# Kernel optimization log

Measured on AMD Instinct MI355X. Metric: run time of the kernel, lower is better.

## Reference

```python
import jax, jax.numpy as jnp
import numpy as np

N, IN_F, H, D = 3072, 512, 8, 64


def setup_inputs() -> dict:
    key = jax.random.key(0)
    k1, k2, k3, k4, k5 = jax.random.split(key, 5)
    x = jax.random.normal(k1, (N, IN_F), dtype=jnp.float32)
    adj = jax.random.randint(k2, (N, N), 0, 2, dtype=jnp.int32)
    # xavier-uniform-like scales
    s_W = (6.0 / (IN_F + H * D)) ** 0.5
    s_a = (6.0 / (H + D)) ** 0.5
    W = jax.random.uniform(k3, (H * D, IN_F), dtype=jnp.float32, minval=-s_W, maxval=s_W)
    a_src = jax.random.uniform(k4, (H, D), dtype=jnp.float32, minval=-s_a, maxval=s_a)
    a_dst = jax.random.uniform(k5, (H, D), dtype=jnp.float32, minval=-s_a, maxval=s_a)
    return {"x": x, "adj": adj, "W": W, "a_src": a_src, "a_dst": a_dst}


def reference(x, adj, W, a_src, a_dst):
    n = x.shape[0]
    Hh, d = a_src.shape
    h = (x @ W.T).reshape(n, Hh, d)                      # [n, H, d]
    e_src = jnp.einsum('nhd,hd->nh', h, a_src)           # [n, H]
    e_dst = jnp.einsum('nhd,hd->nh', h, a_dst)           # [n, H]
    e = e_src[:, None, :] + e_dst[None, :, :]            # [n, n, H], e[i,j]=src_i+dst_j
    e = jax.nn.leaky_relu(e, negative_slope=0.2)
    mask = (adj + jnp.eye(n, dtype=adj.dtype)) > 0       # [n, n]
    e = jnp.where(mask[:, :, None], e, -jnp.inf)
    alpha = jax.nn.softmax(e, axis=1)                    # softmax over j (neighbors)
    # out[i,h,d] = sum_j alpha[i,j,h] * h[j,h,d]  (dropout=0 / eval mode)
    out = jnp.einsum('ijh,jhd->ihd', alpha, h)
    return out.reshape(n, Hh * d)                        # concat=True
```

## Files before the change

kernel.cpp:

```cpp
#include <hip/hip_runtime.h>
#include <hip/hip_bf16.h>

typedef __bf16 bf16x8 __attribute__((ext_vector_type(8)));
typedef _Float16 half8 __attribute__((ext_vector_type(8)));
typedef _Float16 half2v __attribute__((ext_vector_type(2)));
typedef short s16x2 __attribute__((ext_vector_type(2)));
typedef float f32x4 __attribute__((ext_vector_type(4)));
typedef float f32x16 __attribute__((ext_vector_type(16)));

#define NROW 3072
#define NF 512
#define NH 8
#define ND 64
#define BP_BLOCKS 768
#define GEMM_BLOCKS 384

__device__ __forceinline__ unsigned gat_enc_key(float f) {
    unsigned u = __float_as_uint(f);
    return (f < 0.f) ? ~u : (u | 0x80000000u);
}
__device__ __forceinline__ float gat_dec_key(unsigned k) {
    unsigned u = (k & 0x80000000u) ? (k ^ 0x80000000u) : ~k;
    return __uint_as_float(u);
}

__device__ __forceinline__ bf16x8 gat_ld_cvt8(const float* p) {
    float4 f0 = *reinterpret_cast<const float4*>(p);
    float4 f1 = *reinterpret_cast<const float4*>(p + 4);
    bf16x8 o = { (__bf16)f0.x, (__bf16)f0.y, (__bf16)f0.z, (__bf16)f0.w,
                 (__bf16)f1.x, (__bf16)f1.y, (__bf16)f1.z, (__bf16)f1.w };
    return o;
}

__global__ __launch_bounds__(256) void gat_gemm_bp(const float* __restrict__ x,
                                                   const float* __restrict__ W,
                                                   _Float16* __restrict__ hT,
                                                   const int* __restrict__ adj,
                                                   unsigned long long* __restrict__ bits64,
                                                   const float* __restrict__ a_src,
                                                   const float* __restrict__ a_dst,
                                                   float* __restrict__ e_srcT,
                                                   float* __restrict__ e_dstT,
                                                   unsigned* __restrict__ maxkey) {
    __shared__ __align__(16) _Float16 smem[10240];
    __shared__ float ered[2][2][2][32];

    int tid = threadIdx.x;
    int wave = tid >> 6;
    int lane = tid & 63;

    if (blockIdx.x < BP_BLOCKS) {
        int row = blockIdx.x * 4 + wave;
        const int* p = adj + (long)row * NROW + lane;
        int v[48];
#pragma unroll
        for (int s = 0; s < 48; ++s) v[s] = p[s * 64];
        unsigned long long diag = 1ull << (row & 63);
        int dseg = row >> 6;
#pragma unroll
        for (int s = 0; s < 48; ++s) {
            unsigned long long bal = __ballot(v[s] > 0);
            if (s == dseg) bal |= diag;
            if (lane == 0) bits64[(long)row * 48 + s] = bal;
        }
        return;
    }

    int b = blockIdx.x - BP_BLOCKS;
    int i0 = (b >> 3) * 64;
    int o0 = (b & 7) * 64;
    int head = b & 7;
    int half = lane >> 5;
    int l31 = lane & 31;
    int wr = wave >> 1;
    int wc = wave & 1;

    __bf16* sA = reinterpret_cast<__bf16*>(smem);
    __bf16* sB = reinterpret_cast<__bf16*>(smem) + 5120;

    int r = tid >> 2;
    int pp = tid & 3;
    const float* gA = x + (i0 + r) * NF + pp * 8;
    const float* gB = W + (o0 + r) * NF + pp * 8;
    int dslot = r * 40 + pp * 8;

    bf16x8 pA0, pB0, pA1, pB1;
    pA0 = gat_ld_cvt8(gA);
    pB0 = gat_ld_cvt8(gB);
    *reinterpret_cast<bf16x8*>(sA + dslot) = pA0;
    *reinterpret_cast<bf16x8*>(sB + dslot) = pB0;
    pA1 = gat_ld_cvt8(gA + 32);
    pB1 = gat_ld_cvt8(gB + 32);
    __syncthreads();

    f32x16 acc = {};
    int arow = (wr * 32 + l31) * 40;
    int brow = (wc * 32 + l31) * 40;

#pragma unroll
    for (int cc = 0; cc < 8; ++cc) {
        int c0 = cc * 2;
        if (c0 + 2 < 16) {
            pA0 = gat_ld_cvt8(gA + (c0 + 2) * 32);
            pB0 = gat_ld_cvt8(gB + (c0 + 2) * 32);
        }
        {
            const __bf16* pa = sA;
            const __bf16* pb = sB;
#pragma unroll
            for (int ks = 0; ks < 2; ++ks) {
                int q = (((ks << 1) | half)) << 3;
                bf16x8 a = *reinterpret_cast<const bf16x8*>(pa + arow + q);
                bf16x8 bb = *reinterpret_cast<const bf16x8*>(pb + brow + q);
                acc = __builtin_amdgcn_mfma_f32_32x32x16_bf16(a, bb, acc, 0, 0, 0);
            }
        }
        *reinterpret_cast<bf16x8*>(sA + 2560 + dslot) = pA1;
        *reinterpret_cast<bf16x8*>(sB + 2560 + dslot) = pB1;
        __syncthreads();

        int c1 = c0 + 1;
        if (c1 + 2 < 16) {
            pA1 = gat_ld_cvt8(gA + (c1 + 2) * 32);
            pB1 = gat_ld_cvt8(gB + (c1 + 2) * 32);
        }
        {
            const __bf16* pa = sA + 2560;
            const __bf16* pb = sB + 2560;
#pragma unroll
            for (int ks = 0; ks < 2; ++ks) {
                int q = (((ks << 1) | half)) << 3;
                bf16x8 a = *reinterpret_cast<const bf16x8*>(pa + arow + q);
                bf16x8 bb = *reinterpret_cast<const bf16x8*>(pb + brow + q);
                acc = __builtin_amdgcn_mfma_f32_32x32x16_bf16(a, bb, acc, 0, 0, 0);
            }
        }
        if (c1 + 1 < 16) {
            *reinterpret_cast<bf16x8*>(sA + dslot) = pA0;
            *reinterpret_cast<bf16x8*>(sB + dslot) = pB0;
        }
        __syncthreads();
    }

    _Float16* tt = smem + wave * 1280;
#pragma unroll
    for (int reg = 0; reg < 16; ++reg) {
        int rowl = (reg & 3) + 8 * (reg >> 2) + 4 * half;
        tt[rowl * 40 + l31] = (_Float16)acc[reg];
    }
    int orow = lane >> 1;
    int li = (lane & 1) * 16;
    half8 h0, h1;
#pragma unroll
    for (int t = 0; t < 8; ++t) h0[t] = tt[(li + t) * 40 + orow];
#pragma unroll
    for (int t = 0; t < 8; ++t) h1[t] = tt[(li + 8 + t) * 40 + orow];
    _Float16* op = hT + (long)(o0 + wc * 32 + orow) * NROW + i0 + wr * 32 + li;
    *reinterpret_cast<half8*>(op) = h0;
    *reinterpret_cast<half8*>(op + 8) = h1;

    half8 hv0 = *reinterpret_cast<const half8*>(tt + l31 * 40 + half * 16);
    half8 hv1 = *reinterpret_cast<const half8*>(tt + l31 * 40 + half * 16 + 8);
    const float* ap = a_src + head * ND + wc * 32 + half * 16;
    const float* dp = a_dst + head * ND + wc * 32 + half * 16;
    float4 as0 = *reinterpret_cast<const float4*>(ap);
    float4 as1 = *reinterpret_cast<const float4*>(ap + 4);
    float4 as2 = *reinterpret_cast<const float4*>(ap + 8);
    float4 as3 = *reinterpret_cast<const float4*>(ap + 12);
    float4 ad0 = *reinterpret_cast<const float4*>(dp);
    float4 ad1 = *reinterpret_cast<const float4*>(dp + 4);
    float4 ad2 = *reinterpret_cast<const float4*>(dp + 8);
    float4 ad3 = *reinterpret_cast<const float4*>(dp + 12);
    float ps = 0.f, pd = 0.f;
    ps += (float)hv0[0]*as0.x + (float)hv0[1]*as0.y + (float)hv0[2]*as0.z + (float)hv0[3]*as0.w;
    ps += (float)hv0[4]*as1.x + (float)hv0[5]*as1.y + (float)hv0[6]*as1.z + (float)hv0[7]*as1.w;
    ps += (float)hv1[0]*as2.x + (float)hv1[1]*as2.y + (float)hv1[2]*as2.z + (float)hv1[3]*as2.w;
    ps += (float)hv1[4]*as3.x + (float)hv1[5]*as3.y + (float)hv1[6]*as3.z + (float)hv1[7]*as3.w;
    pd += (float)hv0[0]*ad0.x + (float)hv0[1]*ad0.y + (float)hv0[2]*ad0.z + (float)hv0[3]*ad0.w;
    pd += (float)hv0[4]*ad1.x + (float)hv0[5]*ad1.y + (float)hv0[6]*ad1.z + (float)hv0[7]*ad1.w;
    pd += (float)hv1[0]*ad2.x + (float)hv1[1]*ad2.y + (float)hv1[2]*ad2.z + (float)hv1[3]*ad2.w;
    pd += (float)hv1[4]*ad3.x + (float)hv1[5]*ad3.y + (float)hv1[6]*ad3.z + (float)hv1[7]*ad3.w;
    ps += __shfl_xor(ps, 32, 64);
    pd += __shfl_xor(pd, 32, 64);
    if (half == 0) { ered[0][wr][wc][l31] = ps; ered[1][wr][wc][l31] = pd; }
    __syncthreads();
    if (wc == 0) {
        float pst = ered[0][wr][0][l31] + ered[0][wr][1][l31];
        float pdt = ered[1][wr][0][l31] + ered[1][wr][1][l31];
        if (half == 0) {
            e_srcT[head * NROW + i0 + wr * 32 + l31] = pst;
            e_dstT[head * NROW + i0 + wr * 32 + l31] = pdt;
        }
        float mx = pdt;
#pragma unroll
        for (int off = 1; off < 32; off <<= 1) mx = fmaxf(mx, __shfl_xor(mx, off, 64));
        if (lane == 0) atomicMax(&maxkey[head], gat_enc_key(mx));
    }
}

__global__ __launch_bounds__(256) void gat_attn(const unsigned* __restrict__ bits,
                                                const float* __restrict__ e_srcT,
                                                const float* __restrict__ e_dstT,
                                                const unsigned* __restrict__ maxkey,
                                                const _Float16* __restrict__ hT,
                                                _Float16* __restrict__ num,
                                                float* __restrict__ den) {
    constexpr int JCHUNK = NROW / 4;
    constexpr int NC = JCHUNK / 64;
    __shared__ unsigned lds_P[JCHUNK / 2];
    __shared__ unsigned lds_Q[JCHUNK / 2];
    __shared__ __align__(16) _Float16 hbuf[2][4096];
    int b = blockIdx.x;
    int head = b & 7;
    int jc = (b >> 3) & 3;
    int i0 = (b >> 5) * 256;
    int jbase = jc * JCHUNK;
    int tid = threadIdx.x;
    int wave = tid >> 6;
    int lane = tid & 63;
    int half = lane >> 5;
    int l31 = lane & 31;

    float Mg = gat_dec_key(maxkey[head]);
    for (int p = tid; p < JCHUNK / 2; p += 256) {
        float t0 = e_dstT[head * NROW + jbase + 2 * p] - Mg;
        float t1 = e_dstT[head * NROW + jbase + 2 * p + 1] - Mg;
        half2v P = { (_Float16)__expf(t0), (_Float16)__expf(t1) };
        half2v Q = { (_Float16)__expf(0.2f * t0), (_Float16)__expf(0.2f * t1) };
        lds_P[p] = __builtin_bit_cast(unsigned, P);
        lds_Q[p] = __builtin_bit_cast(unsigned, Q);
    }

    int irowA = i0 + wave * 32 + l31;
    int irowB = irowA + 128;
    float uA = e_srcT[head * NROW + irowA] + Mg;
    float uB = e_srcT[head * NROW + irowB] + Mg;
    float RfA = fminf(__expf(-0.8f * uA), 60000.f);
    float RfB = fminf(__expf(-0.8f * uB), 60000.f);
    _Float16 RhA = (_Float16)RfA, RhB = (_Float16)RfB;
    half2v R2A = { RhA, RhA };
    half2v R2B = { RhB, RhB };
    const half8 ones8 = { (_Float16)1.f, (_Float16)1.f, (_Float16)1.f, (_Float16)1.f,
                          (_Float16)1.f, (_Float16)1.f, (_Float16)1.f, (_Float16)1.f };
    const unsigned* browA = bits + (long)irowA * 96 + jc * (JCHUNK / 32);
    const unsigned* browB = bits + (long)irowB * 96 + jc * (JCHUNK / 32);

    int s0 = tid, s1 = tid + 256;
    const _Float16* gp0 = hT + (head * ND + ((s0 >> 6) & 1) * 32 + (s0 & 31)) * NROW
                             + jbase + (s0 >> 7) * 16 + ((s0 >> 5) & 1) * 8;
    const _Float16* gp1 = hT + (head * ND + ((s1 >> 6) & 1) * 32 + (s1 & 31)) * NROW
                             + jbase + (s1 >> 7) * 16 + ((s1 >> 5) & 1) * 8;
    *reinterpret_cast<half8*>(&hbuf[0][tid * 8])         = *reinterpret_cast<const half8*>(gp0);
    *reinterpret_cast<half8*>(&hbuf[0][(tid + 256) * 8]) = *reinterpret_cast<const half8*>(gp1);
    __syncthreads();

    f32x16 acc0a = {}, acc1a = {}, acc2a = {};
    f32x16 acc0b = {}, acc1b = {}, acc2b = {};
    uint2 wmA = *reinterpret_cast<const uint2*>(browA);
    uint2 wmB = *reinterpret_cast<const uint2*>(browB);

    for (int k = 0; k < NC; ++k) {
        half8 st0, st1;
        uint2 wmnA = wmA, wmnB = wmB;
        bool more = (k + 1 < NC);
        if (more) {
            st0 = *reinterpret_cast<const half8*>(gp0 + (k + 1) * 64);
            st1 = *reinterpret_cast<const half8*>(gp1 + (k + 1) * 64);
            wmnA = *reinterpret_cast<const uint2*>(browA + (k + 1) * 2);
            wmnB = *reinterpret_cast<const uint2*>(browB + (k + 1) * 2);
        }
        const _Float16* hb = &hbuf[k & 1][0];
#pragma unroll
        for (int js = 0; js < 4; ++js) {
            int sh = (js & 1) * 16 + half * 8;
            unsigned w8A = (((js < 2) ? wmA.x : wmA.y) >> sh) & 0xffu;
            unsigned w8B = (((js < 2) ? wmB.x : wmB.y) >> sh) & 0xffu;
            unsigned long long S64A = ((unsigned long long)(w8A & 0x55u) << 15)
                                    | ((unsigned long long)(w8A & 0xAAu) << 30);
            unsigned long long S64B = ((unsigned long long)(w8B & 0x55u) << 15)
                                    | ((unsigned long long)(w8B & 0xAAu) << 30);
            uint4 Pv = *reinterpret_cast<const uint4*>(&lds_P[k * 32 + js * 8 + half * 4]);
            uint4 Qv = *reinterpret_cast<const uint4*>(&lds_Q[k * 32 + js * 8 + half * 4]);
            unsigned pr[4] = { Pv.x, Pv.y, Pv.z, Pv.w };
            unsigned qr[4] = { Qv.x, Qv.y, Qv.z, Qv.w };
            unsigned amA[4], amB[4];
#pragma unroll
            for (int t = 0; t < 4; ++t) {
                half2v pv = __builtin_bit_cast(half2v, pr[t]);
                half2v qv = __builtin_bit_cast(half2v, qr[t]);
                half2v mxA = __builtin_elementwise_max(pv, qv * R2A);
                half2v mxB = __builtin_elementwise_max(pv, qv * R2B);
                s16x2 mkA = __builtin_bit_cast(s16x2, (unsigned)(S64A >> (2 * t))) >> 15;
                s16x2 mkB = __builtin_bit_cast(s16x2, (unsigned)(S64B >> (2 * t))) >> 15;
                amA[t] = __builtin_bit_cast(unsigned, mxA) & __builtin_bit_cast(unsigned, mkA);
                amB[t] = __builtin_bit_cast(unsigned, mxB) & __builtin_bit_cast(unsigned, mkB);
            }
            uint4 m4a = { amA[0], amA[1], amA[2], amA[3] };
            uint4 m4b = { amB[0], amB[1], amB[2], amB[3] };
            half8 afA = __builtin_bit_cast(half8, m4a);
            half8 afB = __builtin_bit_cast(half8, m4b);
            half8 v0 = *reinterpret_cast<const half8*>(hb + (js * 128 + lane) * 8);
            half8 v1 = *reinterpret_cast<const half8*>(hb + (js * 128 + 64 + lane) * 8);
            acc0a = __builtin_amdgcn_mfma_f32_32x32x16_f16(afA, v0, acc0a, 0, 0, 0);
            acc1a = __builtin_amdgcn_mfma_f32_32x32x16_f16(afA, v1, acc1a, 0, 0, 0);
            acc2a = __builtin_amdgcn_mfma_f32_32x32x16_f16(afA, ones8, acc2a, 0, 0, 0);
            acc0b = __builtin_amdgcn_mfma_f32_32x32x16_f16(afB, v0, acc0b, 0, 0, 0);
            acc1b = __builtin_amdgcn_mfma_f32_32x32x16_f16(afB, v1, acc1b, 0, 0, 0);
            acc2b = __builtin_amdgcn_mfma_f32_32x32x16_f16(afB, ones8, acc2b, 0, 0, 0);
        }
        if (more) {
            *reinterpret_cast<half8*>(&hbuf[(k + 1) & 1][tid * 8])         = st0;
            *reinterpret_cast<half8*>(&hbuf[(k + 1) & 1][(tid + 256) * 8]) = st1;
        }
        wmA = wmnA;
        wmB = wmnB;
        __syncthreads();
    }

#pragma unroll
    for (int reg = 0; reg < 16; ++reg) {
        int rowl = (reg & 3) + 8 * (reg >> 2) + 4 * half;
        long rbaseA = (long)(jc * NROW + i0 + wave * 32 + rowl);
        long rbaseB = rbaseA + 128;
        if (l31 == 0) {
            den[rbaseA * NH + head] = acc2a[reg];
            den[rbaseB * NH + head] = acc2b[reg];
        }
        long obA = rbaseA * NF + head * ND + l31;
        long obB = rbaseB * NF + head * ND + l31;
        num[obA]      = (_Float16)acc0a[reg];
        num[obA + 32] = (_Float16)acc1a[reg];
        num[obB]      = (_Float16)acc0b[reg];
        num[obB + 32] = (_Float16)acc1b[reg];
    }
}

__global__ __launch_bounds__(256) void gat_final(const _Float16* __restrict__ num,
                                                 const float* __restrict__ den,
                                                 float* __restrict__ out) {
    int idx = (blockIdx.x * 256 + threadIdx.x) * 8;
    int i = idx >> 9;
    int c = idx & 511;
    int head = c >> 6;
    half8 n0 = *reinterpret_cast<const half8*>(num + (long)i * NF + c);
    half8 n1 = *reinterpret_cast<const half8*>(num + (long)(NROW + i) * NF + c);
    half8 n2 = *reinterpret_cast<const half8*>(num + (long)(2 * NROW + i) * NF + c);
    half8 n3 = *reinterpret_cast<const half8*>(num + (long)(3 * NROW + i) * NF + c);
    float ds = den[i * NH + head] + den[(NROW + i) * NH + head]
             + den[(2 * NROW + i) * NH + head] + den[(3 * NROW + i) * NH + head];
    float inv = 1.0f / fmaxf(ds, 1e-30f);
    float r0 = ((float)n0[0] + (float)n1[0] + (float)n2[0] + (float)n3[0]) * inv;
    float r1 = ((float)n0[1] + (float)n1[1] + (float)n2[1] + (float)n3[1]) * inv;
    float r2 = ((float)n0[2] + (float)n1[2] + (float)n2[2] + (float)n3[2]) * inv;
    float r3 = ((float)n0[3] + (float)n1[3] + (float)n2[3] + (float)n3[3]) * inv;
    float r4 = ((float)n0[4] + (float)n1[4] + (float)n2[4] + (float)n3[4]) * inv;
    float r5 = ((float)n0[5] + (float)n1[5] + (float)n2[5] + (float)n3[5]) * inv;
    float r6 = ((float)n0[6] + (float)n1[6] + (float)n2[6] + (float)n3[6]) * inv;
    float r7 = ((float)n0[7] + (float)n1[7] + (float)n2[7] + (float)n3[7]) * inv;
    float4 o0 = { r0, r1, r2, r3 };
    float4 o1 = { r4, r5, r6, r7 };
    *reinterpret_cast<float4*>(out + idx)     = o0;
    *reinterpret_cast<float4*>(out + idx + 4) = o1;
}

extern "C" void kernel_launch(void* const* d_in, const int* in_sizes, int n_in,
                              void* d_out, int out_size, void* d_ws, size_t ws_size,
                              hipStream_t stream) {
    const float* x_raw  = (const float*)d_in[0];
    const int*   adj    = (const int*)d_in[1];
    const float* W_raw  = (const float*)d_in[2];
    const float* as_raw = (const float*)d_in[3];
    const float* ad_raw = (const float*)d_in[4];
    float* out = (float*)d_out;

    char* ws = (char*)d_ws;
    _Float16* hT     = (_Float16*)(ws);
    float*    e_srcT = (float*)(ws + 3145728);
    float*    e_dstT = (float*)(ws + 3244032);
    unsigned* maxkey = (unsigned*)(ws + 3342336);
    unsigned* bits   = (unsigned*)(ws + 3342400);
    _Float16* num    = (_Float16*)(ws + 8192064);
    float*    den    = (float*)(ws + 20774976);

    hipMemsetAsync(maxkey, 0, 64, stream);
    gat_gemm_bp<<<BP_BLOCKS + GEMM_BLOCKS, 256, 0, stream>>>(x_raw, W_raw, hT, adj,
                                                             (unsigned long long*)bits,
                                                             as_raw, ad_raw,
                                                             e_srcT, e_dstT, maxkey);
    gat_attn<<<12 * 4 * 8, 256, 0, stream>>>(bits, e_srcT, e_dstT, maxkey, hT, num, den);
    gat_final<<<NROW * NF / 2048, 256, 0, stream>>>(num, den, out);
}
```

Before: 134.1 us.

## Make the GEMM tile loads per-wave without block barriers and schedule GEMM blocks first

Each wave now loads and converts its own 32-row slices of x and W into a private LDS slab. This removes all __syncthreads from the K loop, and the wave keeps a two-deep register prefetch of float4 loads. GEMM blocks are moved to the front of the grid, so they start before the adjacency bit-packing blocks and the projection is less likely to sit on the tail. In exchange, A and B rows are loaded twice across the waves of a block, which doubles L2 and global traffic for the small GEMM.

```diff
diff --git a/kernel.cpp b/kernel.cpp
--- a/kernel.cpp
+++ b/kernel.cpp
@@ -2,6 +2,7 @@
 #include <hip/hip_bf16.h>
 
 typedef __bf16 bf16x8 __attribute__((ext_vector_type(8)));
+typedef __bf16 bf16x4 __attribute__((ext_vector_type(4)));
 typedef _Float16 half8 __attribute__((ext_vector_type(8)));
 typedef _Float16 half2v __attribute__((ext_vector_type(2)));
 typedef short s16x2 __attribute__((ext_vector_type(2)));
@@ -12,8 +13,8 @@
 #define NF 512
 #define NH 8
 #define ND 64
+#define GEMM_BLOCKS 384
 #define BP_BLOCKS 768
-#define GEMM_BLOCKS 384
 
 __device__ __forceinline__ unsigned gat_enc_key(float f) {
     unsigned u = __float_as_uint(f);
@@ -24,12 +25,27 @@
     return __uint_as_float(u);
 }
 
-__device__ __forceinline__ bf16x8 gat_ld_cvt8(const float* p) {
-    float4 f0 = *reinterpret_cast<const float4*>(p);
-    float4 f1 = *reinterpret_cast<const float4*>(p + 4);
-    bf16x8 o = { (__bf16)f0.x, (__bf16)f0.y, (__bf16)f0.z, (__bf16)f0.w,
-                 (__bf16)f1.x, (__bf16)f1.y, (__bf16)f1.z, (__bf16)f1.w };
-    return o;
+__device__ __forceinline__ void gat_ld4(float4 (&d)[4], const float* g, int c) {
+#pragma unroll
+    for (int t = 0; t < 4; ++t)
+        d[t] = *reinterpret_cast<const float4*>(g + t * 8 * NF + c * 32);
+}
+__device__ __forceinline__ void gat_st4(__bf16* s, const float4 (&v)[4], int wslot) {
+#pragma unroll
+    for (int t = 0; t < 4; ++t) {
+        bf16x4 w = { (__bf16)v[t].x, (__bf16)v[t].y, (__bf16)v[t].z, (__bf16)v[t].w };
+        *reinterpret_cast<bf16x4*>(s + t * 320 + wslot) = w;
+    }
+}
+__device__ __forceinline__ void gat_mfma2(const __bf16* sA, const __bf16* sB,
+                                          int arow, int half, f32x16& acc) {
+#pragma unroll
+    for (int ks = 0; ks < 2; ++ks) {
+        int q = ((ks << 1) | half) << 3;
+        bf16x8 a = *reinterpret_cast<const bf16x8*>(sA + arow + q);
+        bf16x8 b = *reinterpret_cast<const bf16x8*>(sB + arow + q);
+        acc = __builtin_amdgcn_mfma_f32_32x32x16_bf16(a, b, acc, 0, 0, 0);
+    }
 }
 
 __global__ __launch_bounds__(256) void gat_gemm_bp(const float* __restrict__ x,
@@ -49,8 +65,8 @@
     int wave = tid >> 6;
     int lane = tid & 63;
 
-    if (blockIdx.x < BP_BLOCKS) {
-        int row = blockIdx.x * 4 + wave;
+    if (blockIdx.x >= GEMM_BLOCKS) {
+        int row = (blockIdx.x - GEMM_BLOCKS) * 4 + wave;
         const int* p = adj + (long)row * NROW + lane;
         int v[48];
 #pragma unroll
@@ -66,7 +82,7 @@
         return;
     }
 
-    int b = blockIdx.x - BP_BLOCKS;
+    int b = blockIdx.x;
     int i0 = (b >> 3) * 64;
     int o0 = (b & 7) * 64;
     int head = b & 7;
@@ -75,71 +91,35 @@
     int wr = wave >> 1;
     int wc = wave & 1;
 
-    __bf16* sA = reinterpret_cast<__bf16*>(smem);
-    __bf16* sB = reinterpret_cast<__bf16*>(smem) + 5120;
-
-    int r = tid >> 2;
-    int pp = tid & 3;
-    const float* gA = x + (i0 + r) * NF + pp * 8;
-    const float* gB = W + (o0 + r) * NF + pp * 8;
-    int dslot = r * 40 + pp * 8;
-
-    bf16x8 pA0, pB0, pA1, pB1;
-    pA0 = gat_ld_cvt8(gA);
-    pB0 = gat_ld_cvt8(gB);
-    *reinterpret_cast<bf16x8*>(sA + dslot) = pA0;
-    *reinterpret_cast<bf16x8*>(sB + dslot) = pB0;
-    pA1 = gat_ld_cvt8(gA + 32);
-    pB1 = gat_ld_cvt8(gB + 32);
-    __syncthreads();
+    __bf16* sAw = reinterpret_cast<__bf16*>(smem) + wave * 1280;
+    __bf16* sBw = reinterpret_cast<__bf16*>(smem) + 5120 + wave * 1280;
+
+    int lr = lane >> 3;
+    int lc = (lane & 7) * 4;
+    const float* gA = x + (long)(i0 + wr * 32 + lr) * NF + lc;
+    const float* gB = W + (long)(o0 + wc * 32 + lr) * NF + lc;
+    int wslot = lr * 40 + lc;
+
+    float4 Ae[4], Be[4], Ao[4], Bo[4];
+    gat_ld4(Ae, gA, 0); gat_ld4(Be, gB, 0);
+    gat_st4(sAw, Ae, wslot); gat_st4(sBw, Be, wslot);
+    gat_ld4(Ao, gA, 1); gat_ld4(Bo, gB, 1);
+    gat_ld4(Ae, gA, 2); gat_ld4(Be, gB, 2);
 
     f32x16 acc = {};
-    int arow = (wr * 32 + l31) * 40;
-    int brow = (wc * 32 + l31) * 40;
+    int arow = l31 * 40;
 
 #pragma unroll
     for (int cc = 0; cc < 8; ++cc) {
-        int c0 = cc * 2;
-        if (c0 + 2 < 16) {
-            pA0 = gat_ld_cvt8(gA + (c0 + 2) * 32);
-            pB0 = gat_ld_cvt8(gB + (c0 + 2) * 32);
-        }
-        {
-            const __bf16* pa = sA;
-            const __bf16* pb = sB;
-#pragma unroll
-            for (int ks = 0; ks < 2; ++ks) {
-                int q = (((ks << 1) | half)) << 3;
-                bf16x8 a = *reinterpret_cast<const bf16x8*>(pa + arow + q);
-                bf16x8 bb = *reinterpret_cast<const bf16x8*>(pb + brow + q);
-                acc = __builtin_amdgcn_mfma_f32_32x32x16_bf16(a, bb, acc, 0, 0, 0);
-            }
-        }
-        *reinterpret_cast<bf16x8*>(sA + 2560 + dslot) = pA1;
-        *reinterpret_cast<bf16x8*>(sB + 2560 + dslot) = pB1;
-        __syncthreads();
-
-        int c1 = c0 + 1;
-        if (c1 + 2 < 16) {
-            pA1 = gat_ld_cvt8(gA + (c1 + 2) * 32);
-            pB1 = gat_ld_cvt8(gB + (c1 + 2) * 32);
-        }
-        {
-            const __bf16* pa = sA + 2560;
-            const __bf16* pb = sB + 2560;
-#pragma unroll
-            for (int ks = 0; ks < 2; ++ks) {
-                int q = (((ks << 1) | half)) << 3;
-                bf16x8 a = *reinterpret_cast<const bf16x8*>(pa + arow + q);
-                bf16x8 bb = *reinterpret_cast<const bf16x8*>(pb + brow + q);
-                acc = __builtin_amdgcn_mfma_f32_32x32x16_bf16(a, bb, acc, 0, 0, 0);
-            }
-        }
+        int c0 = cc * 2, c1 = c0 + 1;
+        gat_mfma2(sAw, sBw, arow, half, acc);
+        gat_st4(sAw, Ao, wslot); gat_st4(sBw, Bo, wslot);
+        if (c0 + 3 < 16) { gat_ld4(Ao, gA, c0 + 3); gat_ld4(Bo, gB, c0 + 3); }
+        gat_mfma2(sAw, sBw, arow, half, acc);
         if (c1 + 1 < 16) {
-            *reinterpret_cast<bf16x8*>(sA + dslot) = pA0;
-            *reinterpret_cast<bf16x8*>(sB + dslot) = pB0;
-        }
-        __syncthreads();
+            gat_st4(sAw, Ae, wslot); gat_st4(sBw, Be, wslot);
+            if (c1 + 3 < 16) { gat_ld4(Ae, gA, c1 + 3); gat_ld4(Be, gB, c1 + 3); }
+        }
     }
 
     _Float16* tt = smem + wave * 1280;
@@ -383,7 +363,7 @@
     float*    den    = (float*)(ws + 20774976);
 
     hipMemsetAsync(maxkey, 0, 64, stream);
-    gat_gemm_bp<<<BP_BLOCKS + GEMM_BLOCKS, 256, 0, stream>>>(x_raw, W_raw, hT, adj,
+    gat_gemm_bp<<<GEMM_BLOCKS + BP_BLOCKS, 256, 0, stream>>>(x_raw, W_raw, hT, adj,
                                                              (unsigned long long*)bits,
                                                              as_raw, ad_raw,
                                                              e_srcT, e_dstT, maxkey);
```

New measurement: 134.2 us. About the same (+0.1%).
